# Kernel optimization log

Measured on AMD Instinct MI355X. Metric: run time of the kernel, lower is better.

## Reference

```python
import jax, jax.numpy as jnp
import numpy as np

B, N, IN_DIM, HIDDEN, OUT_DIM, HEADS = 4, 2048, 64, 128, 128, 4
NEG_INF = -1e9
EPS = 1e-12  # matches tf.math.l2_normalize epsilon


def setup_inputs() -> dict:
    key = jax.random.key(0)
    ks = jax.random.split(key, 13)
    d1 = HIDDEN // HEADS
    d2 = OUT_DIM // HEADS
    s = lambda k, shape, fan: jax.random.normal(k, shape, jnp.float32) * (1.0 / np.sqrt(fan))
    return {
        "x": jax.random.normal(ks[0], (B, N, IN_DIM), jnp.float32),
        "embedding": s(ks[1], (N, HIDDEN), HIDDEN),
        "Wp": s(ks[2], (IN_DIM, HIDDEN), IN_DIM),
        "bp": jnp.zeros((HIDDEN,), jnp.float32),
        "W1": s(ks[3], (HIDDEN, HIDDEN), HIDDEN),
        "a1_src": s(ks[4], (HEADS, d1), d1),
        "a1_dst": s(ks[5], (HEADS, d1), d1),
        "b1": jnp.zeros((HIDDEN,), jnp.float32),
        "W2": s(ks[6], (HIDDEN, OUT_DIM), HIDDEN),
        "a2_src": s(ks[7], (HEADS, d2), d2),
        "a2_dst": s(ks[8], (HEADS, d2), d2),
        "b2": jnp.zeros((OUT_DIM,), jnp.float32),
    }


def _gat(h, mask, W, a_src, a_dst, b, heads):
    # h: [B,N,F_in], mask: [N,N] bool (adj > 0.5), W: [F_in, heads*d]
    Bn, Nn, _ = h.shape
    d = W.shape[1] // heads
    hh = (h @ W).reshape(Bn, Nn, heads, d)                 # [B,N,H,D]
    s_src = jnp.einsum('bnhd,hd->bnh', hh, a_src)          # score of source node j
    s_dst = jnp.einsum('bnhd,hd->bnh', hh, a_dst)          # score of target node i
    # e[b,i,j,h]: raw attention logit for edge j -> i
    e = jax.nn.leaky_relu(s_dst[:, :, None, :] + s_src[:, None, :, :], 0.2)
    e = jnp.where(mask[None, :, :, None], e, NEG_INF)
    alpha = jax.nn.softmax(e, axis=2)                      # softmax over neighbors j
    out = jnp.einsum('bijh,bjhd->bihd', alpha, hh)         # aggregate messages
    return out.reshape(Bn, Nn, heads * d) + b


def reference(x, embedding, Wp, bp, W1, a1_src, a1_dst, b1, W2, a2_src, a2_dst, b2):
    # AdaptiveAdjacency: cosine similarity of learned node embeddings
    ne = embedding * jax.lax.rsqrt(jnp.sum(embedding * embedding, -1, keepdims=True) + EPS)
    adj = ne @ ne.T                                        # [N,N]
    mask = adj > 0.5                                       # dynamic edge set (diag always True)
    h = x @ Wp + bp                                        # Dense projection
    h = jax.nn.gelu(_gat(h, mask, W1, a1_src, a1_dst, b1, HEADS), approximate=False)
    return _gat(h, mask, W2, a2_src, a2_dst, b2, HEADS)
```

## Files before the change

### kernel.cpp

```cpp
#include <hip/hip_runtime.h>
#include <hip/hip_bf16.h>

using u64 = unsigned long long;

constexpr int Bb    = 4;
constexpr int Nn    = 2048;
constexpr int INDIM = 64;
constexpr int HID   = 128;
constexpr int NW    = Nn / 64;

struct AdjS {
    float As[32][132];
    float Bs[32][68];
    float nA[128];
    float nB[64];
    unsigned char mb[128][8];
};

__global__ __launch_bounds__(256) void k_adjproj(
        const float* __restrict__ emb, u64* __restrict__ maskw,
        const float* __restrict__ x,   const float* __restrict__ Wp,
        const float* __restrict__ bp,  const float* __restrict__ W1,
        const float* __restrict__ a1s, const float* __restrict__ a1d,
        float* __restrict__ hh1, float* __restrict__ s1s, float* __restrict__ s1d) {
    __shared__ __align__(16) unsigned char smem[sizeof(AdjS)];
    const int t = threadIdx.x;

    if (blockIdx.x < 512) {
        AdjS& S = *reinterpret_cast<AdjS*>(smem);
        const int i0 = (blockIdx.x >> 5) * 128;
        const int j0 = (blockIdx.x & 31) * 64;
        const int tx = t & 7, ty = t >> 3;
        const int sra = t >> 1, sha = (t & 1) * 16;
        const int srb = t >> 2, shb = (t & 3) * 8;

        float acc[4][8];
        #pragma unroll
        for (int a = 0; a < 4; ++a)
            #pragma unroll
            for (int b = 0; b < 8; ++b) acc[a][b] = 0.f;

        float sqa = 0.f, sqb = 0.f;

        for (int kc = 0; kc < HID; kc += 32) {
            const float* gA = emb + (size_t)(i0 + sra) * HID + kc + sha;
            const float* gB = emb + (size_t)(j0 + srb) * HID + kc + shb;
            #pragma unroll
            for (int e = 0; e < 16; e += 4) {
                const float4 va = *reinterpret_cast<const float4*>(gA + e);
                S.As[sha + e + 0][sra] = va.x; S.As[sha + e + 1][sra] = va.y;
                S.As[sha + e + 2][sra] = va.z; S.As[sha + e + 3][sra] = va.w;
                sqa += va.x * va.x + va.y * va.y + va.z * va.z + va.w * va.w;
            }
            #pragma unroll
            for (int e = 0; e < 8; e += 4) {
                const float4 vb = *reinterpret_cast<const float4*>(gB + e);
                S.Bs[shb + e + 0][srb] = vb.x; S.Bs[shb + e + 1][srb] = vb.y;
                S.Bs[shb + e + 2][srb] = vb.z; S.Bs[shb + e + 3][srb] = vb.w;
                sqb += vb.x * vb.x + vb.y * vb.y + vb.z * vb.z + vb.w * vb.w;
            }
            __syncthreads();
            #pragma unroll 8
            for (int k = 0; k < 32; ++k) {
                float a[4], b[8];
                *reinterpret_cast<float4*>(a)     = *reinterpret_cast<const float4*>(&S.As[k][ty * 4]);
                *reinterpret_cast<float4*>(&b[0]) = *reinterpret_cast<const float4*>(&S.Bs[k][tx * 8]);
                *reinterpret_cast<float4*>(&b[4]) = *reinterpret_cast<const float4*>(&S.Bs[k][tx * 8 + 4]);
                #pragma unroll
                for (int ii = 0; ii < 4; ++ii)
                    #pragma unroll
                    for (int jj = 0; jj < 8; ++jj)
                        acc[ii][jj] += a[ii] * b[jj];
            }
            __syncthreads();
        }

        {
            const float ta = sqa + __shfl_xor(sqa, 1, 64);
            if ((t & 1) == 0) S.nA[sra] = rsqrtf(ta + 1e-12f);
            float tb = sqb + __shfl_xor(sqb, 1, 64);
            tb += __shfl_xor(tb, 2, 64);
            if ((t & 3) == 0) S.nB[srb] = rsqrtf(tb + 1e-12f);
        }
        __syncthreads();

        float rsj[8];
        #pragma unroll
        for (int jj = 0; jj < 8; ++jj) rsj[jj] = S.nB[tx * 8 + jj];
        #pragma unroll
        for (int e = 0; e < 4; ++e) {
            const float rsi = S.nA[ty * 4 + e];
            unsigned byte = 0;
            #pragma unroll
            for (int jj = 0; jj < 8; ++jj)
                if (acc[e][jj] * rsi * rsj[jj] > 0.5f) byte |= (1u << jj);
            S.mb[ty * 4 + e][tx] = (unsigned char)byte;
        }
        __syncthreads();
        if (t < 128) {
            const u64 bits = *reinterpret_cast<const u64*>(S.mb[t]);
            maskw[(size_t)(i0 + t) * NW + (blockIdx.x & 31)] = bits;
        }
    } else {
        float (*hl)[128] = reinterpret_cast<float(*)[128]>(smem);
        const int h  = t >> 7;
        const int c  = t & 127;
        const int r0 = (blockIdx.x - 512) * 16 + h * 8;

        float acc[8];
        const float bias = bp[c];
        #pragma unroll
        for (int r = 0; r < 8; ++r) acc[r] = bias;
        #pragma unroll 4
        for (int k = 0; k < INDIM; ++k) {
            const float wp = Wp[k * HID + c];
            #pragma unroll
            for (int r = 0; r < 8; ++r)
                acc[r] += x[(size_t)(r0 + r) * INDIM + k] * wp;
        }
        #pragma unroll
        for (int r = 0; r < 8; ++r) hl[h * 8 + r][c] = acc[r];
        __syncthreads();

        float a2[8];
        #pragma unroll
        for (int r = 0; r < 8; ++r) a2[r] = 0.f;
        #pragma unroll 4
        for (int k = 0; k < HID; ++k) {
            const float w = W1[k * HID + c];
            #pragma unroll
            for (int r = 0; r < 8; ++r)
                a2[r] += hl[h * 8 + r][k] * w;
        }
        const float as = a1s[c], ad = a1d[c];
        #pragma unroll
        for (int r = 0; r < 8; ++r) {
            hh1[(size_t)(r0 + r) * HID + c] = a2[r];
            float vs = a2[r] * as;
            float vd = a2[r] * ad;
            #pragma unroll
            for (int m = 1; m < 32; m <<= 1) {
                vs += __shfl_xor(vs, m, 32);
                vd += __shfl_xor(vd, m, 32);
            }
            if ((c & 31) == 0) {
                s1s[(size_t)(r0 + r) * 4 + (c >> 5)] = vs;
                s1d[(size_t)(r0 + r) * 4 + (c >> 5)] = vd;
            }
        }
    }
}

__global__ __launch_bounds__(128) void k_gathid2(
        const float* __restrict__ hh1,
        const float* __restrict__ s1s, const float* __restrict__ s1d,
        const u64* __restrict__ maskw, const float* __restrict__ b1v,
        const float* __restrict__ W2,
        const float* __restrict__ a2s, const float* __restrict__ a2d,
        float* __restrict__ hh2,
        float* __restrict__ s2s, float* __restrict__ s2d) {
    const int r0   = blockIdx.x * 8;
    const int bb   = r0 >> 11;
    const int t    = threadIdx.x;
    const int wv   = t >> 6;
    const int lane = t & 63;
    const int h0   = lane >> 5, h1 = 2 + h0;
    __shared__ float gl[8][128];

    for (int rr = 0; rr < 4; ++rr) {
        const int r   = wv * 4 + rr;
        const int row = r0 + r, i = row & (Nn - 1);
        const u64* mrow = maskw + (size_t)i * NW;
        const u64 myw = (lane < NW) ? mrow[lane] : 0ULL;
        u64 nz = __ballot(myw != 0ULL);
        const float sd0 = s1d[(size_t)row * 4 + h0];
        const float sd1 = s1d[(size_t)row * 4 + h1];
        float m0 = -INFINITY, l0 = 0.f, a0 = 0.f;
        float m1 = -INFINITY, l1 = 0.f, a1 = 0.f;
        while (nz) {
            const int w = __builtin_ctzll(nz); nz &= nz - 1;
            u64 word = __shfl(myw, w, 64);
            while (word) {
                const int bit = __builtin_ctzll(word); word &= word - 1;
                const int jr = (bb << 11) + (w << 6) + bit;
                float e0 = sd0 + s1s[(size_t)jr * 4 + h0];
                e0 = e0 > 0.f ? e0 : 0.2f * e0;
                float e1 = sd1 + s1s[(size_t)jr * 4 + h1];
                e1 = e1 > 0.f ? e1 : 0.2f * e1;
                const float v0 = hh1[(size_t)jr * HID + lane];
                const float v1 = hh1[(size_t)jr * HID + 64 + lane];
                float nm = fmaxf(m0, e0);
                float sc = __expf(m0 - nm);
                float p  = __expf(e0 - nm);
                l0 = l0 * sc + p; a0 = a0 * sc + p * v0; m0 = nm;
                nm = fmaxf(m1, e1);
                sc = __expf(m1 - nm);
                p  = __expf(e1 - nm);
                l1 = l1 * sc + p; a1 = a1 * sc + p * v1; m1 = nm;
            }
        }
        float o0 = (l0 > 0.f ? a0 / l0 : 0.f) + b1v[lane];
        float o1 = (l1 > 0.f ? a1 / l1 : 0.f) + b1v[64 + lane];
        o0 = 0.5f * o0 * (1.f + erff(o0 * 0.70710678118654752f));
        o1 = 0.5f * o1 * (1.f + erff(o1 * 0.70710678118654752f));
        gl[r][lane]      = o0;
        gl[r][64 + lane] = o1;
    }
    __syncthreads();

    const int c = t;
    float acc[8];
    #pragma unroll
    for (int r = 0; r < 8; ++r) acc[r] = 0.f;
    #pragma unroll 4
    for (int k = 0; k < HID; ++k) {
        const float w = W2[k * HID + c];
        #pragma unroll
        for (int r = 0; r < 8; ++r)
            acc[r] += gl[r][k] * w;
    }
    const float as = a2s[c], ad = a2d[c];
    #pragma unroll
    for (int r = 0; r < 8; ++r) {
        hh2[(size_t)(r0 + r) * HID + c] = acc[r];
        float vs = acc[r] * as;
        float vd = acc[r] * ad;
        #pragma unroll
        for (int m = 1; m < 32; m <<= 1) {
            vs += __shfl_xor(vs, m, 32);
            vd += __shfl_xor(vd, m, 32);
        }
        if ((c & 31) == 0) {
            s2s[(size_t)(r0 + r) * 4 + (c >> 5)] = vs;
            s2d[(size_t)(r0 + r) * 4 + (c >> 5)] = vd;
        }
    }
}

__global__ __launch_bounds__(64) void k_gat(const float* __restrict__ hh,
                                            const float* __restrict__ ssrc,
                                            const float* __restrict__ sdst,
                                            const u64* __restrict__ maskw,
                                            const float* __restrict__ bias,
                                            float* __restrict__ out) {
    const int row  = blockIdx.x;
    const int i    = row & (Nn - 1);
    const int b    = row >> 11;
    const int lane = threadIdx.x;
    const int h0   = lane >> 5;
    const int h1   = 2 + h0;
    const float sd0 = sdst[(size_t)row * 4 + h0];
    const float sd1 = sdst[(size_t)row * 4 + h1];
    const u64* mrow = maskw + (size_t)i * NW;

    const u64 myw = (lane < NW) ? mrow[lane] : 0ULL;
    u64 nz = __ballot(myw != 0ULL);

    float m0 = -INFINITY, l0 = 0.f, a0 = 0.f;
    float m1 = -INFINITY, l1 = 0.f, a1 = 0.f;

    while (nz) {
        const int w = __builtin_ctzll(nz); nz &= nz - 1;
        u64 word = __shfl(myw, w, 64);
        while (word) {
            const int bit = __builtin_ctzll(word); word &= word - 1;
            const int jr = (b << 11) + (w << 6) + bit;
            float e0 = sd0 + ssrc[(size_t)jr * 4 + h0];
            e0 = e0 > 0.f ? e0 : 0.2f * e0;
            float e1 = sd1 + ssrc[(size_t)jr * 4 + h1];
            e1 = e1 > 0.f ? e1 : 0.2f * e1;
            const float v0 = hh[(size_t)jr * HID + lane];
            const float v1 = hh[(size_t)jr * HID + 64 + lane];
            float nm = fmaxf(m0, e0);
            float sc = __expf(m0 - nm);
            float p  = __expf(e0 - nm);
            l0 = l0 * sc + p; a0 = a0 * sc + p * v0; m0 = nm;
            nm = fmaxf(m1, e1);
            sc = __expf(m1 - nm);
            p  = __expf(e1 - nm);
            l1 = l1 * sc + p; a1 = a1 * sc + p * v1; m1 = nm;
        }
    }

    out[(size_t)row * HID + lane]      = (l0 > 0.f ? a0 / l0 : 0.f) + bias[lane];
    out[(size_t)row * HID + 64 + lane] = (l1 > 0.f ? a1 / l1 : 0.f) + bias[64 + lane];
}

extern "C" void kernel_launch(void* const* d_in, const int* in_sizes, int n_in,
                              void* d_out, int out_size, void* d_ws, size_t ws_size,
                              hipStream_t stream) {
    const float* x   = (const float*)d_in[0];
    const float* emb = (const float*)d_in[1];
    const float* Wp  = (const float*)d_in[2];
    const float* bp  = (const float*)d_in[3];
    const float* W1  = (const float*)d_in[4];
    const float* a1s = (const float*)d_in[5];
    const float* a1d = (const float*)d_in[6];
    const float* b1  = (const float*)d_in[7];
    const float* W2  = (const float*)d_in[8];
    const float* a2s = (const float*)d_in[9];
    const float* a2d = (const float*)d_in[10];
    const float* b2  = (const float*)d_in[11];

    char* ws = (char*)d_ws;
    u64*  maskw = (u64*)ws;   ws += (size_t)Nn * NW * 8;
    float* hh1  = (float*)ws; ws += (size_t)Bb * Nn * HID * 4;
    float* hh2  = (float*)ws; ws += (size_t)Bb * Nn * HID * 4;
    float* s1s  = (float*)ws; ws += (size_t)Bb * Nn * 4 * 4;
    float* s1d  = (float*)ws; ws += (size_t)Bb * Nn * 4 * 4;
    float* s2s  = (float*)ws; ws += (size_t)Bb * Nn * 4 * 4;
    float* s2d  = (float*)ws; ws += (size_t)Bb * Nn * 4 * 4;

    k_adjproj<<<1024, 256, 0, stream>>>(emb, maskw, x, Wp, bp, W1, a1s, a1d,
                                        hh1, s1s, s1d);
    k_gathid2<<<Bb * Nn / 8, 128, 0, stream>>>(hh1, s1s, s1d, maskw, b1,
                                               W2, a2s, a2d, hh2, s2s, s2d);
    k_gat<<<Bb * Nn, 64, 0, stream>>>(hh2, s2s, s2d, maskw, b2, (float*)d_out);
}
```

Before: 51.20 us.

## Fuse layer-1 aggregation, W2 projection and layer-2 attention into one kernel

Replaces the separate layer-1 aggregation/W2 kernel and the layer-2 GAT kernel with one kernel. For each target row it walks the neighbour list and recomputes, for every neighbour j, the layer-1 attention aggregate, GELU, W2 projection and layer-2 score, then folds them into an online softmax. This drops the hh2/s2 intermediate buffers and one kernel launch. The cost is recomputation that grows with the square of node degree, which stays cheap only while the learned adjacency is very sparse.

```diff
diff --git a/kernel.cpp b/kernel.cpp
--- a/kernel.cpp
+++ b/kernel.cpp
@@ -151,139 +151,98 @@
     }
 }
 
-__global__ __launch_bounds__(128) void k_gathid2(
+__global__ __launch_bounds__(128) void k_layer2(
         const float* __restrict__ hh1,
         const float* __restrict__ s1s, const float* __restrict__ s1d,
         const u64* __restrict__ maskw, const float* __restrict__ b1v,
         const float* __restrict__ W2,
         const float* __restrict__ a2s, const float* __restrict__ a2d,
-        float* __restrict__ hh2,
-        float* __restrict__ s2s, float* __restrict__ s2d) {
-    const int r0   = blockIdx.x * 8;
-    const int bb   = r0 >> 11;
-    const int t    = threadIdx.x;
-    const int wv   = t >> 6;
-    const int lane = t & 63;
-    const int h0   = lane >> 5, h1 = 2 + h0;
-    __shared__ float gl[8][128];
-
-    for (int rr = 0; rr < 4; ++rr) {
-        const int r   = wv * 4 + rr;
-        const int row = r0 + r, i = row & (Nn - 1);
-        const u64* mrow = maskw + (size_t)i * NW;
-        const u64 myw = (lane < NW) ? mrow[lane] : 0ULL;
-        u64 nz = __ballot(myw != 0ULL);
-        const float sd0 = s1d[(size_t)row * 4 + h0];
-        const float sd1 = s1d[(size_t)row * 4 + h1];
-        float m0 = -INFINITY, l0 = 0.f, a0 = 0.f;
-        float m1 = -INFINITY, l1 = 0.f, a1 = 0.f;
-        while (nz) {
-            const int w = __builtin_ctzll(nz); nz &= nz - 1;
-            u64 word = __shfl(myw, w, 64);
-            while (word) {
-                const int bit = __builtin_ctzll(word); word &= word - 1;
-                const int jr = (bb << 11) + (w << 6) + bit;
-                float e0 = sd0 + s1s[(size_t)jr * 4 + h0];
-                e0 = e0 > 0.f ? e0 : 0.2f * e0;
-                float e1 = sd1 + s1s[(size_t)jr * 4 + h1];
-                e1 = e1 > 0.f ? e1 : 0.2f * e1;
-                const float v0 = hh1[(size_t)jr * HID + lane];
-                const float v1 = hh1[(size_t)jr * HID + 64 + lane];
-                float nm = fmaxf(m0, e0);
-                float sc = __expf(m0 - nm);
-                float p  = __expf(e0 - nm);
-                l0 = l0 * sc + p; a0 = a0 * sc + p * v0; m0 = nm;
-                nm = fmaxf(m1, e1);
-                sc = __expf(m1 - nm);
-                p  = __expf(e1 - nm);
-                l1 = l1 * sc + p; a1 = a1 * sc + p * v1; m1 = nm;
-            }
-        }
-        float o0 = (l0 > 0.f ? a0 / l0 : 0.f) + b1v[lane];
-        float o1 = (l1 > 0.f ? a1 / l1 : 0.f) + b1v[64 + lane];
-        o0 = 0.5f * o0 * (1.f + erff(o0 * 0.70710678118654752f));
-        o1 = 0.5f * o1 * (1.f + erff(o1 * 0.70710678118654752f));
-        gl[r][lane]      = o0;
-        gl[r][64 + lane] = o1;
+        const float* __restrict__ b2v,
+        float* __restrict__ out) {
+    const int r0  = blockIdx.x * 8;
+    const int bb  = r0 >> 11;
+    const int c   = threadIdx.x;
+    const int l64 = c & 63;
+    const int hd  = c >> 5;
+    __shared__ float gl[128];
+
+    for (int r = 0; r < 8; ++r) {
+        const int row  = r0 + r;
+        const int iloc = row & (Nn - 1);
+        const u64* mri = maskw + (size_t)iloc * NW;
+        const u64 myi = (l64 < NW) ? mri[l64] : 0ULL;
+        u64 nzi = __ballot(myi != 0ULL);
+
+        float m = -INFINITY, l = 0.f, acc = 0.f;
+        float s2d_i = 0.f;
+
+        int  jloc  = iloc;
+        bool first = true;
+        u64  word  = 0;
+        int  wcur  = 0;
+
+        while (true) {
+            {
+                const int jr = (bb << 11) + jloc;
+                const u64* mrj = maskw + (size_t)jloc * NW;
+                const u64 myj = (l64 < NW) ? mrj[l64] : 0ULL;
+                u64 nzj = __ballot(myj != 0ULL);
+                const float sd = s1d[(size_t)jr * 4 + hd];
+                float m1 = -INFINITY, l1 = 0.f, a1 = 0.f;
+                while (nzj) {
+                    const int w = __builtin_ctzll(nzj); nzj &= nzj - 1;
+                    u64 wd = __shfl(myj, w, 64);
+                    while (wd) {
+                        const int bit = __builtin_ctzll(wd); wd &= wd - 1;
+                        const int j2 = (bb << 11) + (w << 6) + bit;
+                        float e = sd + s1s[(size_t)j2 * 4 + hd];
+                        e = e > 0.f ? e : 0.2f * e;
+                        const float v = hh1[(size_t)j2 * HID + c];
+                        const float nm = fmaxf(m1, e);
+                        const float sc = __expf(m1 - nm);
+                        const float p  = __expf(e - nm);
+                        l1 = l1 * sc + p; a1 = a1 * sc + p * v; m1 = nm;
+                    }
+                }
+                float o = (l1 > 0.f ? a1 / l1 : 0.f) + b1v[c];
+                o = 0.5f * o * (1.f + erff(o * 0.70710678118654752f));
+                __syncthreads();
+                gl[c] = o;
+                __syncthreads();
+            }
+            float val = 0.f;
+            #pragma unroll 4
+            for (int k = 0; k < HID; ++k)
+                val += gl[k] * W2[k * HID + c];
+            float vs = val * a2s[c];
+            #pragma unroll
+            for (int mm = 1; mm < 32; mm <<= 1) vs += __shfl_xor(vs, mm, 32);
+            if (first) {
+                float vd = val * a2d[c];
+                #pragma unroll
+                for (int mm = 1; mm < 32; mm <<= 1) vd += __shfl_xor(vd, mm, 32);
+                s2d_i = vd;
+            }
+            float e = s2d_i + vs;
+            e = e > 0.f ? e : 0.2f * e;
+            const float nm = fmaxf(m, e);
+            const float sc = __expf(m - nm);
+            const float p  = __expf(e - nm);
+            l = l * sc + p; acc = acc * sc + p * val; m = nm;
+
+            if (first) { first = false; word = 0; }
+            while (word == 0) {
+                if (nzi == 0) break;
+                wcur = __builtin_ctzll(nzi); nzi &= nzi - 1;
+                word = __shfl(myi, wcur, 64);
+                if (wcur == (iloc >> 6)) word &= ~(1ULL << (iloc & 63));
+            }
+            if (word == 0) break;
+            const int bit = __builtin_ctzll(word); word &= word - 1;
+            jloc = (wcur << 6) + bit;
+        }
+        out[(size_t)row * HID + c] = acc / l + b2v[c];
     }
-    __syncthreads();
-
-    const int c = t;
-    float acc[8];
-    #pragma unroll
-    for (int r = 0; r < 8; ++r) acc[r] = 0.f;
-    #pragma unroll 4
-    for (int k = 0; k < HID; ++k) {
-        const float w = W2[k * HID + c];
-        #pragma unroll
-        for (int r = 0; r < 8; ++r)
-            acc[r] += gl[r][k] * w;
-    }
-    const float as = a2s[c], ad = a2d[c];
-    #pragma unroll
-    for (int r = 0; r < 8; ++r) {
-        hh2[(size_t)(r0 + r) * HID + c] = acc[r];
-        float vs = acc[r] * as;
-        float vd = acc[r] * ad;
-        #pragma unroll
-        for (int m = 1; m < 32; m <<= 1) {
-            vs += __shfl_xor(vs, m, 32);
-            vd += __shfl_xor(vd, m, 32);
-        }
-        if ((c & 31) == 0) {
-            s2s[(size_t)(r0 + r) * 4 + (c >> 5)] = vs;
-            s2d[(size_t)(r0 + r) * 4 + (c >> 5)] = vd;
-        }
-    }
-}
-
-__global__ __launch_bounds__(64) void k_gat(const float* __restrict__ hh,
-                                            const float* __restrict__ ssrc,
-                                            const float* __restrict__ sdst,
-                                            const u64* __restrict__ maskw,
-                                            const float* __restrict__ bias,
-                                            float* __restrict__ out) {
-    const int row  = blockIdx.x;
-    const int i    = row & (Nn - 1);
-    const int b    = row >> 11;
-    const int lane = threadIdx.x;
-    const int h0   = lane >> 5;
-    const int h1   = 2 + h0;
-    const float sd0 = sdst[(size_t)row * 4 + h0];
-    const float sd1 = sdst[(size_t)row * 4 + h1];
-    const u64* mrow = maskw + (size_t)i * NW;
-
-    const u64 myw = (lane < NW) ? mrow[lane] : 0ULL;
-    u64 nz = __ballot(myw != 0ULL);
-
-    float m0 = -INFINITY, l0 = 0.f, a0 = 0.f;
-    float m1 = -INFINITY, l1 = 0.f, a1 = 0.f;
-
-    while (nz) {
-        const int w = __builtin_ctzll(nz); nz &= nz - 1;
-        u64 word = __shfl(myw, w, 64);
-        while (word) {
-            const int bit = __builtin_ctzll(word); word &= word - 1;
-            const int jr = (b << 11) + (w << 6) + bit;
-            float e0 = sd0 + ssrc[(size_t)jr * 4 + h0];
-            e0 = e0 > 0.f ? e0 : 0.2f * e0;
-            float e1 = sd1 + ssrc[(size_t)jr * 4 + h1];
-            e1 = e1 > 0.f ? e1 : 0.2f * e1;
-            const float v0 = hh[(size_t)jr * HID + lane];
-            const float v1 = hh[(size_t)jr * HID + 64 + lane];
-            float nm = fmaxf(m0, e0);
-            float sc = __expf(m0 - nm);
-            float p  = __expf(e0 - nm);
-            l0 = l0 * sc + p; a0 = a0 * sc + p * v0; m0 = nm;
-            nm = fmaxf(m1, e1);
-            sc = __expf(m1 - nm);
-            p  = __expf(e1 - nm);
-            l1 = l1 * sc + p; a1 = a1 * sc + p * v1; m1 = nm;
-        }
-    }
-
-    out[(size_t)row * HID + lane]      = (l0 > 0.f ? a0 / l0 : 0.f) + bias[lane];
-    out[(size_t)row * HID + 64 + lane] = (l1 > 0.f ? a1 / l1 : 0.f) + bias[64 + lane];
 }
 
 extern "C" void kernel_launch(void* const* d_in, const int* in_sizes, int n_in,
@@ -305,15 +264,11 @@
     char* ws = (char*)d_ws;
     u64*  maskw = (u64*)ws;   ws += (size_t)Nn * NW * 8;
     float* hh1  = (float*)ws; ws += (size_t)Bb * Nn * HID * 4;
-    float* hh2  = (float*)ws; ws += (size_t)Bb * Nn * HID * 4;
     float* s1s  = (float*)ws; ws += (size_t)Bb * Nn * 4 * 4;
     float* s1d  = (float*)ws; ws += (size_t)Bb * Nn * 4 * 4;
-    float* s2s  = (float*)ws; ws += (size_t)Bb * Nn * 4 * 4;
-    float* s2d  = (float*)ws; ws += (size_t)Bb * Nn * 4 * 4;
 
     k_adjproj<<<1024, 256, 0, stream>>>(emb, maskw, x, Wp, bp, W1, a1s, a1d,
                                         hh1, s1s, s1d);
-    k_gathid2<<<Bb * Nn / 8, 128, 0, stream>>>(hh1, s1s, s1d, maskw, b1,
-                                               W2, a2s, a2d, hh2, s2s, s2d);
-    k_gat<<<Bb * Nn, 64, 0, stream>>>(hh2, s2s, s2d, maskw, b2, (float*)d_out);
+    k_layer2<<<Bb * Nn / 8, 128, 0, stream>>>(hh1, s1s, s1d, maskw, b1,
+                                              W2, a2s, a2d, b2, (float*)d_out);
 }
```

Measured after the change: 73.20 us. +43.0%, slower.

## Exploit adjacency symmetry by computing only upper-triangular 64x64 tiles

Applied to the files above, without the earlier changes.

The cosine-similarity adjacency is symmetric, so the mask kernel now computes only the upper-triangular 64x64 tiles (528 blocks instead of 512 blocks of 128x64) and writes each off-diagonal tile's bits both directly and transposed. This roughly halves the FLOPs and embedding loads for the adjacency GEMM. In exchange, tiles are smaller and so get less register reuse, a serial loop maps block index to tile, and extra shared-memory bit packing is needed for the transpose. Floating-point rounding could make mask bits at exact symmetric threshold cases differ from the reference, which computes both orders.

```diff
diff --git a/kernel.cpp b/kernel.cpp
--- a/kernel.cpp
+++ b/kernel.cpp
@@ -8,13 +8,16 @@
 constexpr int INDIM = 64;
 constexpr int HID   = 128;
 constexpr int NW    = Nn / 64;
+constexpr int NT    = 32;
+constexpr int NTRI  = NT * (NT + 1) / 2;
 
 struct AdjS {
-    float As[32][132];
+    float As[32][68];
     float Bs[32][68];
-    float nA[128];
+    float nA[64];
     float nB[64];
-    unsigned char mb[128][8];
+    unsigned char mb [64][16];
+    unsigned char mbT[64][16];
 };
 
 __global__ __launch_bounds__(256) void k_adjproj(
@@ -26,86 +29,108 @@
     __shared__ __align__(16) unsigned char smem[sizeof(AdjS)];
     const int t = threadIdx.x;
 
-    if (blockIdx.x < 512) {
+    if (blockIdx.x < NTRI) {
         AdjS& S = *reinterpret_cast<AdjS*>(smem);
-        const int i0 = (blockIdx.x >> 5) * 128;
-        const int j0 = (blockIdx.x & 31) * 64;
-        const int tx = t & 7, ty = t >> 3;
-        const int sra = t >> 1, sha = (t & 1) * 16;
-        const int srb = t >> 2, shb = (t & 3) * 8;
-
-        float acc[4][8];
+        int b = blockIdx.x, ti = 0, cum = 0;
+        while (cum + (NT - ti) <= b) { cum += NT - ti; ++ti; }
+        const int tj = ti + (b - cum);
+        const bool diag = (ti == tj);
+        const int i0 = ti * 64, j0 = tj * 64;
+
+        const int tx = t & 15, ty = t >> 4;
+        const int sr = t >> 2, sh = (t & 3) * 8;
+
+        float acc[4][4];
         #pragma unroll
         for (int a = 0; a < 4; ++a)
             #pragma unroll
-            for (int b = 0; b < 8; ++b) acc[a][b] = 0.f;
+            for (int c = 0; c < 4; ++c) acc[a][c] = 0.f;
 
         float sqa = 0.f, sqb = 0.f;
 
         for (int kc = 0; kc < HID; kc += 32) {
-            const float* gA = emb + (size_t)(i0 + sra) * HID + kc + sha;
-            const float* gB = emb + (size_t)(j0 + srb) * HID + kc + shb;
-            #pragma unroll
-            for (int e = 0; e < 16; e += 4) {
+            const float* gA = emb + (size_t)(i0 + sr) * HID + kc + sh;
+            const float* gB = emb + (size_t)(j0 + sr) * HID + kc + sh;
+            #pragma unroll
+            for (int e = 0; e < 8; e += 4) {
                 const float4 va = *reinterpret_cast<const float4*>(gA + e);
-                S.As[sha + e + 0][sra] = va.x; S.As[sha + e + 1][sra] = va.y;
-                S.As[sha + e + 2][sra] = va.z; S.As[sha + e + 3][sra] = va.w;
+                const float4 vb = *reinterpret_cast<const float4*>(gB + e);
+                S.As[sh + e + 0][sr] = va.x; S.As[sh + e + 1][sr] = va.y;
+                S.As[sh + e + 2][sr] = va.z; S.As[sh + e + 3][sr] = va.w;
                 sqa += va.x * va.x + va.y * va.y + va.z * va.z + va.w * va.w;
-            }
-            #pragma unroll
-            for (int e = 0; e < 8; e += 4) {
-                const float4 vb = *reinterpret_cast<const float4*>(gB + e);
-                S.Bs[shb + e + 0][srb] = vb.x; S.Bs[shb + e + 1][srb] = vb.y;
-                S.Bs[shb + e + 2][srb] = vb.z; S.Bs[shb + e + 3][srb] = vb.w;
+                S.Bs[sh + e + 0][sr] = vb.x; S.Bs[sh + e + 1][sr] = vb.y;
+                S.Bs[sh + e + 2][sr] = vb.z; S.Bs[sh + e + 3][sr] = vb.w;
                 sqb += vb.x * vb.x + vb.y * vb.y + vb.z * vb.z + vb.w * vb.w;
             }
             __syncthreads();
             #pragma unroll 8
             for (int k = 0; k < 32; ++k) {
-                float a[4], b[8];
-                *reinterpret_cast<float4*>(a)     = *reinterpret_cast<const float4*>(&S.As[k][ty * 4]);
-                *reinterpret_cast<float4*>(&b[0]) = *reinterpret_cast<const float4*>(&S.Bs[k][tx * 8]);
-                *reinterpret_cast<float4*>(&b[4]) = *reinterpret_cast<const float4*>(&S.Bs[k][tx * 8 + 4]);
+                float a[4], c[4];
+                *reinterpret_cast<float4*>(a) = *reinterpret_cast<const float4*>(&S.As[k][ty * 4]);
+                *reinterpret_cast<float4*>(c) = *reinterpret_cast<const float4*>(&S.Bs[k][tx * 4]);
                 #pragma unroll
                 for (int ii = 0; ii < 4; ++ii)
                     #pragma unroll
-                    for (int jj = 0; jj < 8; ++jj)
-                        acc[ii][jj] += a[ii] * b[jj];
+                    for (int jj = 0; jj < 4; ++jj)
+                        acc[ii][jj] += a[ii] * c[jj];
             }
             __syncthreads();
         }
 
         {
-            const float ta = sqa + __shfl_xor(sqa, 1, 64);
-            if ((t & 1) == 0) S.nA[sra] = rsqrtf(ta + 1e-12f);
+            float ta = sqa + __shfl_xor(sqa, 1, 64);
+            ta += __shfl_xor(ta, 2, 64);
+            if ((t & 3) == 0) S.nA[sr] = rsqrtf(ta + 1e-12f);
             float tb = sqb + __shfl_xor(sqb, 1, 64);
             tb += __shfl_xor(tb, 2, 64);
-            if ((t & 3) == 0) S.nB[srb] = rsqrtf(tb + 1e-12f);
+            if ((t & 3) == 0) S.nB[sr] = rsqrtf(tb + 1e-12f);
         }
         __syncthreads();
 
-        float rsj[8];
-        #pragma unroll
-        for (int jj = 0; jj < 8; ++jj) rsj[jj] = S.nB[tx * 8 + jj];
+        float rsi[4], rsj[4];
+        #pragma unroll
+        for (int e = 0; e < 4; ++e) { rsi[e] = S.nA[ty * 4 + e]; rsj[e] = S.nB[tx * 4 + e]; }
+
+        bool bit[4][4];
+        #pragma unroll
+        for (int e = 0; e < 4; ++e)
+            #pragma unroll
+            for (int jj = 0; jj < 4; ++jj)
+                bit[e][jj] = (acc[e][jj] * rsi[e] * rsj[jj] > 0.5f);
+
         #pragma unroll
         for (int e = 0; e < 4; ++e) {
-            const float rsi = S.nA[ty * 4 + e];
-            unsigned byte = 0;
-            #pragma unroll
-            for (int jj = 0; jj < 8; ++jj)
-                if (acc[e][jj] * rsi * rsj[jj] > 0.5f) byte |= (1u << jj);
-            S.mb[ty * 4 + e][tx] = (unsigned char)byte;
+            unsigned nib = 0;
+            #pragma unroll
+            for (int jj = 0; jj < 4; ++jj) if (bit[e][jj]) nib |= (1u << jj);
+            S.mb[ty * 4 + e][tx] = (unsigned char)nib;
+        }
+        #pragma unroll
+        for (int jj = 0; jj < 4; ++jj) {
+            unsigned nib = 0;
+            #pragma unroll
+            for (int e = 0; e < 4; ++e) if (bit[e][jj]) nib |= (1u << e);
+            S.mbT[tx * 4 + jj][ty] = (unsigned char)nib;
         }
         __syncthreads();
-        if (t < 128) {
-            const u64 bits = *reinterpret_cast<const u64*>(S.mb[t]);
-            maskw[(size_t)(i0 + t) * NW + (blockIdx.x & 31)] = bits;
+
+        if (t < 64) {
+            u64 bits = 0;
+            #pragma unroll
+            for (int p = 0; p < 16; ++p) bits |= (u64)S.mb[t][p] << (4 * p);
+            maskw[(size_t)(i0 + t) * NW + tj] = bits;
+        } else if (t < 128 && !diag) {
+            const int c = t - 64;
+            u64 bits = 0;
+            #pragma unroll
+            for (int p = 0; p < 16; ++p) bits |= (u64)S.mbT[c][p] << (4 * p);
+            maskw[(size_t)(j0 + c) * NW + ti] = bits;
         }
     } else {
         float (*hl)[128] = reinterpret_cast<float(*)[128]>(smem);
         const int h  = t >> 7;
         const int c  = t & 127;
-        const int r0 = (blockIdx.x - 512) * 16 + h * 8;
+        const int r0 = (blockIdx.x - NTRI) * 16 + h * 8;
 
         float acc[8];
         const float bias = bp[c];
@@ -311,8 +336,8 @@
     float* s2s  = (float*)ws; ws += (size_t)Bb * Nn * 4 * 4;
     float* s2d  = (float*)ws; ws += (size_t)Bb * Nn * 4 * 4;
 
-    k_adjproj<<<1024, 256, 0, stream>>>(emb, maskw, x, Wp, bp, W1, a1s, a1d,
-                                        hh1, s1s, s1d);
+    k_adjproj<<<NTRI + 512, 256, 0, stream>>>(emb, maskw, x, Wp, bp, W1, a1s, a1d,
+                                              hh1, s1s, s1d);
     k_gathid2<<<Bb * Nn / 8, 128, 0, stream>>>(hh1, s1s, s1d, maskw, b1,
                                                W2, a2s, a2d, hh2, s2s, s2d);
     k_gat<<<Bb * Nn, 64, 0, stream>>>(hh2, s2s, s2d, maskw, b2, (float*)d_out);
```

Result: no change. 51.81 us (+1.2%).
